# Kernel tuning notes

Measured on AMD Instinct MI355X. Metric: run time of the kernel, lower is better.

Reference implementation:

```python
import jax, jax.numpy as jnp
import numpy as np

N_HEAD = 16


def setup_inputs() -> dict:
    key = jax.random.key(0)
    k1, k2, k3 = jax.random.split(key, 3)
    B, T, C = 2, 2048, 1024
    x = jax.random.normal(k1, (B, T, C), dtype=jnp.float32)
    w_attn = jax.random.normal(k2, (C, 3 * C), dtype=jnp.float32) * 0.02
    w_proj = jax.random.normal(k3, (C, C), dtype=jnp.float32) * 0.02
    return {"x": x, "w_attn": w_attn, "w_proj": w_proj}


def reference(x, w_attn, w_proj):
    B, T, C = x.shape
    H = N_HEAD
    D = C // H
    qkv = x @ w_attn  # [B, T, 3C]
    q, k, v = jnp.split(qkv, 3, axis=2)
    q = q.reshape(B, T, H, D)
    k = k.reshape(B, T, H, D)
    v = v.reshape(B, T, H, D)
    scale = 1.0 / jnp.sqrt(jnp.asarray(D, dtype=x.dtype))
    # Full T x T score matrix, matching the 'standard_attention' path.
    att = jnp.einsum('bthd,bshd->bhts', q, k) * scale  # [B, H, T, T]
    causal = jnp.tril(jnp.ones((T, T), dtype=bool))
    att = jnp.where(causal[None, None, :, :], att, jnp.asarray(-jnp.inf, dtype=att.dtype))
    att = jax.nn.softmax(att, axis=-1)
    # dropout_p is False (== 0.0) in the original module, so no dropout applied.
    y = jnp.einsum('bhts,bshd->bthd', att, v)  # [B, T, H, D]
    y = y.reshape(B, T, C)
    return y @ w_proj
```

## Files before the change

### kernel.cpp

```cpp
#include <hip/hip_runtime.h>
#include <math.h>

#define BB 2
#define TT 2048
#define HH 16
#define DD 64
#define CC 1024
#define C3 3072

typedef __attribute__((ext_vector_type(8))) short bf16x8;
typedef __attribute__((ext_vector_type(4))) short bf16x4;
typedef __attribute__((ext_vector_type(4))) float f32x4;
typedef __attribute__((ext_vector_type(2))) unsigned int u32x2;

__device__ __forceinline__ unsigned short f2bf(float f) {
  union { float f; unsigned u; } v; v.f = f;
  unsigned r = v.u + 0x7fffu + ((v.u >> 16) & 1u);
  return (unsigned short)(r >> 16);
}
__device__ __forceinline__ unsigned short f2bf_up(float f) {
  union { float f; unsigned u; } v; v.f = f;
  return (unsigned short)((v.u + 0x8000u) >> 16);
}

__device__ __forceinline__ void async_cp16(const void* g, void* l) {
  __builtin_amdgcn_global_load_lds(
      (const __attribute__((address_space(1))) void*)g,
      (__attribute__((address_space(3))) void*)l, 16, 0, 0);
}

__global__ __launch_bounds__(256)
void prep(const float* __restrict__ x, const float* __restrict__ w_attn,
          const float* __restrict__ w_proj, unsigned short* __restrict__ xb,
          unsigned short* __restrict__ wat, unsigned short* __restrict__ wpt) {
  __shared__ __align__(16) float Ts[64][68];
  const int bx = blockIdx.x, tid = threadIdx.x;
  if (bx < 1024) {
    int i = bx * 256 + tid;
#pragma unroll
    for (int it = 0; it < 4; ++it, i += 262144) {
      const float4 v = ((const float4*)x)[i];
      bf16x4 o = {(short)f2bf(v.x), (short)f2bf(v.y),
                  (short)f2bf(v.z), (short)f2bf(v.w)};
      ((bf16x4*)xb)[i] = o;
    }
    return;
  }
  const float* W;
  unsigned short* WT;
  int Nd, bound, n0, k0;
  float s;
  if (bx < 1792) {
    const int bid = bx - 1024;
    W = w_attn; WT = wat; Nd = 3072; bound = 1024; s = 0.18033688f;
    n0 = (bid % 48) * 64; k0 = (bid / 48) * 64;
  } else {
    const int bid = bx - 1792;
    W = w_proj; WT = wpt; Nd = 1024; bound = 0; s = 1.0f;
    n0 = (bid % 16) * 64; k0 = (bid / 16) * 64;
  }
  const int rl = tid >> 4, c4 = tid & 15;
#pragma unroll
  for (int it = 0; it < 4; ++it) {
    const int r = it * 16 + rl;
    *(float4*)&Ts[r][c4 * 4] =
        *(const float4*)(W + (size_t)(k0 + r) * Nd + n0 + c4 * 4);
  }
  __syncthreads();
#pragma unroll
  for (int it = 0; it < 4; ++it) {
    const int n = it * 16 + rl;
    const float sc = (n0 + n < bound) ? s : 1.0f;
    bf16x4 o = {(short)f2bf(Ts[c4 * 4 + 0][n] * sc),
                (short)f2bf(Ts[c4 * 4 + 1][n] * sc),
                (short)f2bf(Ts[c4 * 4 + 2][n] * sc),
                (short)f2bf(Ts[c4 * 4 + 3][n] * sc)};
    *(bf16x4*)(WT + (size_t)(n0 + n) * CC + k0 + c4 * 4) = o;
  }
}

__global__ __launch_bounds__(256, 2)
void gemm_qkv(const unsigned short* __restrict__ A,
              const unsigned short* __restrict__ BT,
              unsigned short* __restrict__ Cb,
              unsigned short* __restrict__ Vout) {
  __shared__ __align__(16) unsigned short As[2 * 128 * 32];
  __shared__ __align__(16) unsigned short Bs[2 * 192 * 32];

  const int tid = threadIdx.x;
  const int w = tid >> 6, lane = tid & 63;
  const int l15 = lane & 15, quad = lane >> 4;
  const int row0 = blockIdx.y * 128, col0 = blockIdx.x * 192;

  const int ca0 = tid, ca1 = tid + 256;
  const int ra0 = ca0 >> 2, ka0 = ((ca0 & 3) ^ ((ca0 >> 3) & 3)) * 8;
  const int ra1 = ca1 >> 2, ka1 = ((ca1 & 3) ^ ((ca1 >> 3) & 3)) * 8;
  const unsigned short* gA0 = A + (size_t)(row0 + ra0) * CC + ka0;
  const unsigned short* gA1 = A + (size_t)(row0 + ra1) * CC + ka1;
  const int cb0 = tid, cb1 = tid + 256, cb2 = tid + 512;
  const int rb0 = cb0 >> 2, kb0 = ((cb0 & 3) ^ ((cb0 >> 3) & 3)) * 8;
  const int rb1 = cb1 >> 2, kb1 = ((cb1 & 3) ^ ((cb1 >> 3) & 3)) * 8;
  const int rb2 = cb2 >> 2, kb2 = ((cb2 & 3) ^ ((cb2 >> 3) & 3)) * 8;
  const unsigned short* gB0 = BT + (size_t)(col0 + rb0) * CC + kb0;
  const unsigned short* gB1 = BT + (size_t)(col0 + rb1) * CC + kb1;
  const unsigned short* gB2 = BT + (size_t)(col0 + rb2) * CC + kb2;
  const int la0 = tid * 16, la1 = tid * 16 + 4096;
  const int lb0 = tid * 16, lb1 = tid * 16 + 4096, lb2 = tid * 16 + 8192;

  const int fro = l15 * 64 + 16 * (quad ^ ((l15 >> 1) & 3));

  f32x4 acc[8][3];
#pragma unroll
  for (int i = 0; i < 8; ++i)
#pragma unroll
    for (int j = 0; j < 3; ++j) acc[i][j] = (f32x4){0.f, 0.f, 0.f, 0.f};

  async_cp16(gA0, (char*)As + la0);
  async_cp16(gA1, (char*)As + la1);
  async_cp16(gB0, (char*)Bs + lb0);
  async_cp16(gB1, (char*)Bs + lb1);
  async_cp16(gB2, (char*)Bs + lb2);

  for (int i = 0; i < 32; ++i) {
    const int cur = i & 1;
    __syncthreads();

    if (i + 1 < 32) {
      const int k1 = (i + 1) * 32;
      const int ab = (cur ^ 1) * 8192, bb = (cur ^ 1) * 12288;
      async_cp16(gA0 + k1, (char*)As + ab + la0);
      async_cp16(gA1 + k1, (char*)As + ab + la1);
      async_cp16(gB0 + k1, (char*)Bs + bb + lb0);
      async_cp16(gB1 + k1, (char*)Bs + bb + lb1);
      async_cp16(gB2 + k1, (char*)Bs + bb + lb2);
    }

    const char* fA = (const char*)As + cur * 8192 + fro;
    const char* fB = (const char*)Bs + cur * 12288 + w * 3072 + fro;

    bf16x8 af[8], bf[3];
#pragma unroll
    for (int mt = 0; mt < 8; ++mt) af[mt] = *(const bf16x8*)(fA + mt * 1024);
#pragma unroll
    for (int nt = 0; nt < 3; ++nt) bf[nt] = *(const bf16x8*)(fB + nt * 1024);
#pragma unroll
    for (int mt = 0; mt < 8; ++mt)
#pragma unroll
      for (int nt = 0; nt < 3; ++nt)
        acc[mt][nt] = __builtin_amdgcn_mfma_f32_16x16x32_bf16(
            af[mt], bf[nt], acc[mt][nt], 0, 0, 0);
  }

#pragma unroll
  for (int mt = 0; mt < 8; ++mt) {
    const int rbase = row0 + mt * 16 + quad * 4;
#pragma unroll
    for (int nt = 0; nt < 3; ++nt) {
      const int colb = col0 + w * 48 + nt * 16;
      if (colb >= 2048) {
        const int bq = rbase >> 11, t0 = rbase & 2047;
        const int d = colb + l15 - 2048;
        bf16x4 o = {(short)f2bf(acc[mt][nt][0]), (short)f2bf(acc[mt][nt][1]),
                    (short)f2bf(acc[mt][nt][2]), (short)f2bf(acc[mt][nt][3])};
        *(bf16x4*)(Vout + (((size_t)(bq << 10) + d) << 11) + t0) = o;
      } else {
        const int col = colb + l15;
#pragma unroll
        for (int r = 0; r < 4; ++r)
          Cb[(size_t)(rbase + r) * C3 + col] = f2bf(acc[mt][nt][r]);
      }
    }
  }
}

__global__ __launch_bounds__(256, 2)
void gemm_out(const unsigned short* __restrict__ A,
              const unsigned short* __restrict__ BT,
              float* __restrict__ Cf) {
  __shared__ __align__(16) unsigned short As[2 * 64 * 64];
  __shared__ __align__(16) unsigned short Bs[2 * 128 * 64];

  const int tid = threadIdx.x;
  const int w = tid >> 6, lane = tid & 63;
  const int l15 = lane & 15, quad = lane >> 4;
  const int wm = w >> 1, wn = w & 1;
  const int row0 = blockIdx.y * 64, col0 = blockIdx.x * 128;

  const int ca0 = tid, ca1 = tid + 256;
  const int ra0 = ca0 >> 3, ka0 = ((ca0 & 7) ^ ((ca0 >> 3) & 7)) * 8;
  const int ra1 = ca1 >> 3, ka1 = ((ca1 & 7) ^ ((ca1 >> 3) & 7)) * 8;
  const unsigned short* gA0 = A + (size_t)(row0 + ra0) * CC + ka0;
  const unsigned short* gA1 = A + (size_t)(row0 + ra1) * CC + ka1;
  const unsigned short* gB[4];
  int lb[4];
#pragma unroll
  for (int t = 0; t < 4; ++t) {
    const int c = tid + t * 256;
    const int rb = c >> 3, kb = ((c & 7) ^ ((c >> 3) & 7)) * 8;
    gB[t] = BT + (size_t)(col0 + rb) * CC + kb;
    lb[t] = c * 16;
  }
  const int la0 = tid * 16, la1 = tid * 16 + 4096;

  const int fro = l15 * 128 + ((quad ^ (l15 & 7)) << 4);

  f32x4 acc[2][4];
#pragma unroll
  for (int i = 0; i < 2; ++i)
#pragma unroll
    for (int j = 0; j < 4; ++j) acc[i][j] = (f32x4){0.f, 0.f, 0.f, 0.f};

  async_cp16(gA0, (char*)As + la0);
  async_cp16(gA1, (char*)As + la1);
#pragma unroll
  for (int t = 0; t < 4; ++t) async_cp16(gB[t], (char*)Bs + lb[t]);

  for (int i = 0; i < 16; ++i) {
    const int cur = i & 1;
    __syncthreads();

    if (i + 1 < 16) {
      const int k1 = (i + 1) * 64;
      const int ab = (cur ^ 1) * 8192, bb = (cur ^ 1) * 16384;
      async_cp16(gA0 + k1, (char*)As + ab + la0);
      async_cp16(gA1 + k1, (char*)As + ab + la1);
#pragma unroll
      for (int t = 0; t < 4; ++t) async_cp16(gB[t] + k1, (char*)Bs + bb + lb[t]);
    }

    const char* fA = (const char*)As + cur * 8192 + wm * 4096 + fro;
    const char* fB = (const char*)Bs + cur * 16384 + wn * 8192 + fro;

#pragma unroll
    for (int kh = 0; kh < 2; ++kh) {
      const int xo = kh * 64;
      bf16x8 af[2], bf[4];
#pragma unroll
      for (int mt = 0; mt < 2; ++mt)
        af[mt] = *(const bf16x8*)(fA + mt * 2048 + ((fro + xo) & 127) - (fro & 127));
#pragma unroll
      for (int nt = 0; nt < 4; ++nt)
        bf[nt] = *(const bf16x8*)(fB + nt * 2048 + ((fro + xo) & 127) - (fro & 127));
#pragma unroll
      for (int mt = 0; mt < 2; ++mt)
#pragma unroll
        for (int nt = 0; nt < 4; ++nt)
          acc[mt][nt] = __builtin_amdgcn_mfma_f32_16x16x32_bf16(
              af[mt], bf[nt], acc[mt][nt], 0, 0, 0);
    }
  }

#pragma unroll
  for (int mt = 0; mt < 2; ++mt) {
    const int rbase = row0 + wm * 32 + mt * 16 + quad * 4;
#pragma unroll
    for (int r = 0; r < 4; ++r) {
      float* cr = Cf + (size_t)(rbase + r) * CC + col0 + wn * 64 + l15;
#pragma unroll
      for (int nt = 0; nt < 4; ++nt) cr[nt * 16] = acc[mt][nt][r];
    }
  }
}

__global__ __launch_bounds__(256)
void attn_mfma(const unsigned short* __restrict__ qkvb,
               const unsigned short* __restrict__ vt,
               unsigned short* __restrict__ y) {
  const int n = blockIdx.x;
  const int bh = (n & 7) + 8 * ((n >> 3) & 3);
  const int qpair = n >> 5;
  const int b = bh >> 4, h = bh & 15;
  const int tid = threadIdx.x;
  const int w = tid >> 6;
  const int lane = tid & 63;
  const int l15 = lane & 15, quad = lane >> 4;

  __shared__ __align__(16) char Kb[2 * 8192];
  __shared__ __align__(16) char Vb[2 * 8192];
  __shared__ __align__(16) unsigned short Ps[4 * 16 * 72];
  unsigned short* psw = Ps + w * 16 * 72;

  const int lr = lane >> 3;
  const int lc = lane & 7;
  const int srcoff = ((lc ^ lr) << 4);
  const char* ksrc = (const char*)qkvb + ((size_t)(b * TT) * C3 + 1024 + h * 64) * 2;
  const char* vsrc = (const char*)vt + ((size_t)(b * HH + h) * DD * TT) * 2;

  const int fro = l15 * 128 + ((quad ^ (l15 & 7)) << 4);

  bf16x8 onesf;
#pragma unroll
  for (int jj = 0; jj < 8; ++jj) onesf[jj] = (short)0x3F80;

  for (int phase = 0; phase < 2; ++phase) {
    const int qt = phase == 0 ? 31 - qpair : qpair;

    if (phase) __syncthreads();

    const unsigned short* qrow =
        qkvb + (size_t)(b * TT + qt * 64 + w * 16 + l15) * C3 + h * DD;
    bf16x8 qf0 = *(const bf16x8*)(qrow + quad * 8);
    bf16x8 qf1 = *(const bf16x8*)(qrow + 32 + quad * 8);

    f32x4 O[4];
#pragma unroll
    for (int dt = 0; dt < 4; ++dt) O[dt] = (f32x4){0.f, 0.f, 0.f, 0.f};
    f32x4 lacc = (f32x4){0.f, 0.f, 0.f, 0.f};

#pragma unroll
    for (int i = 0; i < 2; ++i) {
      async_cp16(ksrc + (size_t)(w * 16 + i * 8 + lr) * (C3 * 2) + srcoff,
                 Kb + w * 2048 + i * 1024);
      async_cp16(vsrc + (size_t)(w * 16 + i * 8 + lr) * (TT * 2) + srcoff,
                 Vb + w * 2048 + i * 1024);
    }

    for (int j = 0; j <= qt; ++j) {
      const int cur = j & 1;
      __syncthreads();

      if (j < qt) {
        const int key1 = (j + 1) * 64;
        char* kd = Kb + (cur ^ 1) * 8192 + w * 2048;
        char* vd = Vb + (cur ^ 1) * 8192 + w * 2048;
#pragma unroll
        for (int i = 0; i < 2; ++i) {
          async_cp16(
              ksrc + (size_t)(key1 + w * 16 + i * 8 + lr) * (C3 * 2) + srcoff,
              kd + i * 1024);
          async_cp16(
              vsrc + (size_t)(w * 16 + i * 8 + lr) * (TT * 2) + key1 * 2 + srcoff,
              vd + i * 1024);
        }
      }

      const char* Kc = Kb + cur * 8192;
      const char* Vc = Vb + cur * 8192;

      f32x4 S[4];
#pragma unroll
      for (int ct = 0; ct < 4; ++ct) {
        bf16x8 k0 = *(const bf16x8*)(Kc + ct * 2048 + fro);
        bf16x8 k1 = *(const bf16x8*)(Kc + ct * 2048 + (fro ^ 64));
        f32x4 z = (f32x4){-12.f, -12.f, -12.f, -12.f};
        z = __builtin_amdgcn_mfma_f32_16x16x32_bf16(k0, qf0, z, 0, 0, 0);
        z = __builtin_amdgcn_mfma_f32_16x16x32_bf16(k1, qf1, z, 0, 0, 0);
        S[ct] = z;
      }

      if (j == qt) {
#pragma unroll
        for (int ct = 0; ct < 4; ++ct)
#pragma unroll
          for (int r = 0; r < 4; ++r)
            if (16 * ct + quad * 4 + r > w * 16 + l15) S[ct][r] = -INFINITY;
      }

#pragma unroll
      for (int ct = 0; ct < 4; ++ct) {
        const unsigned p0 = f2bf_up(exp2f(S[ct][0]));
        const unsigned p1 = f2bf_up(exp2f(S[ct][1]));
        const unsigned p2 = f2bf_up(exp2f(S[ct][2]));
        const unsigned p3 = f2bf_up(exp2f(S[ct][3]));
        u32x2 d;
        d[0] = p0 | (p1 << 16);
        d[1] = p2 | (p3 << 16);
        *(u32x2*)((char*)psw + l15 * 144 + ct * 32 + quad * 8) = d;
      }

      bf16x8 pf0 = *(const bf16x8*)((char*)psw + l15 * 144 + quad * 16);
      bf16x8 pf1 = *(const bf16x8*)((char*)psw + l15 * 144 + 64 + quad * 16);

      lacc = __builtin_amdgcn_mfma_f32_16x16x32_bf16(onesf, pf0, lacc, 0, 0, 0);
      lacc = __builtin_amdgcn_mfma_f32_16x16x32_bf16(onesf, pf1, lacc, 0, 0, 0);
#pragma unroll
      for (int dt = 0; dt < 4; ++dt) {
        bf16x8 v0 = *(const bf16x8*)(Vc + dt * 2048 + fro);
        bf16x8 v1 = *(const bf16x8*)(Vc + dt * 2048 + (fro ^ 64));
        O[dt] = __builtin_amdgcn_mfma_f32_16x16x32_bf16(v0, pf0, O[dt], 0, 0, 0);
        O[dt] = __builtin_amdgcn_mfma_f32_16x16x32_bf16(v1, pf1, O[dt], 0, 0, 0);
      }
    }

    const float inv = 1.0f / lacc[0];
    unsigned short* yr =
        y + (size_t)(b * TT + qt * 64 + w * 16 + l15) * CC + h * DD + quad * 4;
#pragma unroll
    for (int dt = 0; dt < 4; ++dt) {
      bf16x4 o = {(short)f2bf(O[dt][0] * inv), (short)f2bf(O[dt][1] * inv),
                  (short)f2bf(O[dt][2] * inv), (short)f2bf(O[dt][3] * inv)};
      *(bf16x4*)(yr + dt * 16) = o;
    }
  }
}

extern "C" void kernel_launch(void* const* d_in, const int* in_sizes, int n_in,
                              void* d_out, int out_size, void* d_ws,
                              size_t ws_size, hipStream_t stream) {
  const float* x      = (const float*)d_in[0];
  const float* w_attn = (const float*)d_in[1];
  const float* w_proj = (const float*)d_in[2];
  float* out = (float*)d_out;

  unsigned short* xb   = (unsigned short*)d_ws;
  unsigned short* wat  = xb + (size_t)4096 * 1024;
  unsigned short* wpt  = wat + (size_t)3072 * 1024;
  unsigned short* qkvb = wpt + (size_t)1024 * 1024;
  unsigned short* vt   = qkvb + (size_t)4096 * 3072;
  unsigned short* yb   = vt + (size_t)BB * HH * DD * TT;

  dim3 blk(256);

  prep<<<2048, blk, 0, stream>>>(x, w_attn, w_proj, xb, wat, wpt);

  gemm_qkv<<<dim3(C3 / 192, (BB * TT) / 128), blk, 0, stream>>>(
      xb, wat, qkvb, vt);

  attn_mfma<<<dim3(512, 1, 1), blk, 0, stream>>>(qkvb, vt, yb);

  gemm_out<<<dim3(CC / 128, (BB * TT) / 64), blk, 0, stream>>>(yb, wpt, out);
}
```

Baseline: 184.1 us.

## Software-pipeline QK^T one tile ahead, swizzle P smem, packed bf16 convert

Restructures the attention inner loop so the QK^T scores for the next key tile are computed while softmax-exp and PV of the current tile proceed, with K loads issued two tiles ahead and V one tile ahead. The intent is to overlap MFMA work with exp/convert and hide LDS/global latency. The P scratch layout in shared memory is also swizzled per row to reduce bank conflicts, and the bf16 packing now uses the round-to-nearest paired intrinsic instead of manual round-up. The change raises register pressure from holding two score sets and alters rounding slightly.

Result: no change. 186.1 us (+1.1%).

```diff
diff --git a/kernel.cpp b/kernel.cpp
--- a/kernel.cpp
+++ b/kernel.cpp
@@ -1,4 +1,5 @@
 #include <hip/hip_runtime.h>
+#include <hip/hip_bf16.h>
 #include <math.h>
 
 #define BB 2
@@ -18,9 +19,10 @@
   unsigned r = v.u + 0x7fffu + ((v.u >> 16) & 1u);
   return (unsigned short)(r >> 16);
 }
-__device__ __forceinline__ unsigned short f2bf_up(float f) {
-  union { float f; unsigned u; } v; v.f = f;
-  return (unsigned short)((v.u + 0x8000u) >> 16);
+__device__ __forceinline__ unsigned pack2bf(float a, float b) {
+  __hip_bfloat162 h = __float22bfloat162_rn(make_float2(a, b));
+  union { __hip_bfloat162 h; unsigned u; } cv; cv.h = h;
+  return cv.u;
 }
 
 __device__ __forceinline__ void async_cp16(const void* g, void* l) {
@@ -278,7 +280,7 @@
   __shared__ __align__(16) char Kb[2 * 8192];
   __shared__ __align__(16) char Vb[2 * 8192];
   __shared__ __align__(16) unsigned short Ps[4 * 16 * 72];
-  unsigned short* psw = Ps + w * 16 * 72;
+  char* psw = (char*)(Ps + w * 16 * 72);
 
   const int lr = lane >> 3;
   const int lc = lane & 7;
@@ -288,6 +290,8 @@
 
   const int fro = l15 * 128 + ((quad ^ (l15 & 7)) << 4);
 
+  const int psrow = l15 * 144;
+
   bf16x8 onesf;
 #pragma unroll
   for (int jj = 0; jj < 8; ++jj) onesf[jj] = (short)0x3F80;
@@ -314,30 +318,17 @@
       async_cp16(vsrc + (size_t)(w * 16 + i * 8 + lr) * (TT * 2) + srcoff,
                  Vb + w * 2048 + i * 1024);
     }
-
-    for (int j = 0; j <= qt; ++j) {
-      const int cur = j & 1;
-      __syncthreads();
-
-      if (j < qt) {
-        const int key1 = (j + 1) * 64;
-        char* kd = Kb + (cur ^ 1) * 8192 + w * 2048;
-        char* vd = Vb + (cur ^ 1) * 8192 + w * 2048;
-#pragma unroll
-        for (int i = 0; i < 2; ++i) {
-          async_cp16(
-              ksrc + (size_t)(key1 + w * 16 + i * 8 + lr) * (C3 * 2) + srcoff,
-              kd + i * 1024);
-          async_cp16(
-              vsrc + (size_t)(w * 16 + i * 8 + lr) * (TT * 2) + key1 * 2 + srcoff,
-              vd + i * 1024);
-        }
-      }
-
-      const char* Kc = Kb + cur * 8192;
-      const char* Vc = Vb + cur * 8192;
-
-      f32x4 S[4];
+    if (qt >= 1) {
+#pragma unroll
+      for (int i = 0; i < 2; ++i)
+        async_cp16(ksrc + (size_t)(64 + w * 16 + i * 8 + lr) * (C3 * 2) + srcoff,
+                   Kb + 8192 + w * 2048 + i * 1024);
+    }
+    __syncthreads();
+
+    f32x4 Scur[4];
+    {
+      const char* Kc = Kb;
 #pragma unroll
       for (int ct = 0; ct < 4; ++ct) {
         bf16x8 k0 = *(const bf16x8*)(Kc + ct * 2048 + fro);
@@ -345,40 +336,88 @@
         f32x4 z = (f32x4){-12.f, -12.f, -12.f, -12.f};
         z = __builtin_amdgcn_mfma_f32_16x16x32_bf16(k0, qf0, z, 0, 0, 0);
         z = __builtin_amdgcn_mfma_f32_16x16x32_bf16(k1, qf1, z, 0, 0, 0);
-        S[ct] = z;
-      }
-
-      if (j == qt) {
+        Scur[ct] = z;
+      }
+      if (qt == 0) {
 #pragma unroll
         for (int ct = 0; ct < 4; ++ct)
 #pragma unroll
           for (int r = 0; r < 4; ++r)
-            if (16 * ct + quad * 4 + r > w * 16 + l15) S[ct][r] = -INFINITY;
+            if (16 * ct + quad * 4 + r > w * 16 + l15) Scur[ct][r] = -INFINITY;
+      }
+    }
+
+    for (int j = 0; j <= qt; ++j) {
+      __syncthreads();
+
+      if (j + 2 <= qt) {
+        const int keyk = (j + 2) * 64;
+        char* kd = Kb + (j & 1) * 8192 + w * 2048;
+#pragma unroll
+        for (int i = 0; i < 2; ++i)
+          async_cp16(ksrc + (size_t)(keyk + w * 16 + i * 8 + lr) * (C3 * 2) + srcoff,
+                     kd + i * 1024);
+      }
+      if (j + 1 <= qt) {
+        const int keyv = (j + 1) * 64;
+        char* vd = Vb + ((j + 1) & 1) * 8192 + w * 2048;
+#pragma unroll
+        for (int i = 0; i < 2; ++i)
+          async_cp16(vsrc + (size_t)(w * 16 + i * 8 + lr) * (TT * 2) + keyv * 2 + srcoff,
+                     vd + i * 1024);
+      }
+
+      f32x4 Snxt[4];
+      const bool have_nxt = (j + 1 <= qt);
+      if (have_nxt) {
+        const char* Kc = Kb + ((j + 1) & 1) * 8192;
+#pragma unroll
+        for (int ct = 0; ct < 4; ++ct) {
+          bf16x8 k0 = *(const bf16x8*)(Kc + ct * 2048 + fro);
+          bf16x8 k1 = *(const bf16x8*)(Kc + ct * 2048 + (fro ^ 64));
+          f32x4 z = (f32x4){-12.f, -12.f, -12.f, -12.f};
+          z = __builtin_amdgcn_mfma_f32_16x16x32_bf16(k0, qf0, z, 0, 0, 0);
+          z = __builtin_amdgcn_mfma_f32_16x16x32_bf16(k1, qf1, z, 0, 0, 0);
+          Snxt[ct] = z;
+        }
+        if (j + 1 == qt) {
+#pragma unroll
+          for (int ct = 0; ct < 4; ++ct)
+#pragma unroll
+            for (int r = 0; r < 4; ++r)
+              if (16 * ct + quad * 4 + r > w * 16 + l15) Snxt[ct][r] = -INFINITY;
+        }
       }
 
 #pragma unroll
       for (int ct = 0; ct < 4; ++ct) {
-        const unsigned p0 = f2bf_up(exp2f(S[ct][0]));
-        const unsigned p1 = f2bf_up(exp2f(S[ct][1]));
-        const unsigned p2 = f2bf_up(exp2f(S[ct][2]));
-        const unsigned p3 = f2bf_up(exp2f(S[ct][3]));
         u32x2 d;
-        d[0] = p0 | (p1 << 16);
-        d[1] = p2 | (p3 << 16);
-        *(u32x2*)((char*)psw + l15 * 144 + ct * 32 + quad * 8) = d;
-      }
-
-      bf16x8 pf0 = *(const bf16x8*)((char*)psw + l15 * 144 + quad * 16);
-      bf16x8 pf1 = *(const bf16x8*)((char*)psw + l15 * 144 + 64 + quad * 16);
+        d[0] = pack2bf(exp2f(Scur[ct][0]), exp2f(Scur[ct][1]));
+        d[1] = pack2bf(exp2f(Scur[ct][2]), exp2f(Scur[ct][3]));
+        *(u32x2*)(psw + psrow + (((ct + l15) & 3) << 5) + quad * 8) = d;
+      }
+
+      bf16x8 pf0, pf1;
+      {
+        const int c0 = (quad >> 1), c1 = 2 + (quad >> 1);
+        pf0 = *(const bf16x8*)(psw + psrow + (((c0 + l15) & 3) << 5) + ((quad & 1) << 4));
+        pf1 = *(const bf16x8*)(psw + psrow + (((c1 + l15) & 3) << 5) + ((quad & 1) << 4));
+      }
 
       lacc = __builtin_amdgcn_mfma_f32_16x16x32_bf16(onesf, pf0, lacc, 0, 0, 0);
       lacc = __builtin_amdgcn_mfma_f32_16x16x32_bf16(onesf, pf1, lacc, 0, 0, 0);
+      const char* Vc = Vb + (j & 1) * 8192;
 #pragma unroll
       for (int dt = 0; dt < 4; ++dt) {
         bf16x8 v0 = *(const bf16x8*)(Vc + dt * 2048 + fro);
         bf16x8 v1 = *(const bf16x8*)(Vc + dt * 2048 + (fro ^ 64));
         O[dt] = __builtin_amdgcn_mfma_f32_16x16x32_bf16(v0, pf0, O[dt], 0, 0, 0);
         O[dt] = __builtin_amdgcn_mfma_f32_16x16x32_bf16(v1, pf1, O[dt], 0, 0, 0);
+      }
+
+      if (have_nxt) {
+#pragma unroll
+        for (int ct = 0; ct < 4; ++ct) Scur[ct] = Snxt[ct];
       }
     }
 
```
